# Kernel tuning notes

Hardware: AMD Instinct MI355X
Metric: run time of the kernel (lower is better)

The kernel has to match this reference:

```python
import jax, jax.numpy as jnp
import numpy as np

N_ATOM = 4_000_000
N_FRAG = 200_000
EIG_THRESHOLD = 0.01


def setup_inputs() -> dict:
    key = jax.random.key(0)
    k1, k2, k3, k4, k5 = jax.random.split(key, 5)
    f_atom = jax.random.normal(k1, (N_ATOM, 3), jnp.float32)
    atom_pos = jax.random.normal(k2, (N_ATOM, 3), jnp.float32) * 5.0
    T_frag = jax.random.normal(k3, (N_FRAG, 3), jnp.float32) * 5.0
    frag_id = jax.random.randint(k4, (N_ATOM,), 0, N_FRAG)
    frag_sizes = jax.random.randint(k5, (N_FRAG,), 1, 40)
    return {"f_atom": f_atom, "atom_pos": atom_pos, "T_frag": T_frag,
            "frag_id": frag_id, "frag_sizes": frag_sizes, "n_frag": N_FRAG}


def reference(f_atom, atom_pos, T_frag, frag_id, frag_sizes, n_frag):
    dtype = f_atom.dtype
    # scatter_mean(f_atom, frag_id): segment_sum / counts
    counts = jax.ops.segment_sum(jnp.ones((f_atom.shape[0],), dtype), frag_id,
                                 num_segments=n_frag)
    denom = jnp.maximum(counts, 1.0)[:, None]
    v_frag = jax.ops.segment_sum(f_atom, frag_id, num_segments=n_frag) / denom  # [F,3]

    r_arm = atom_pos - T_frag[frag_id]                                   # [N,3]
    torque = jax.ops.segment_sum(jnp.cross(r_arm, f_atom), frag_id,
                                 num_segments=n_frag)                    # [F,3]

    r2 = jnp.sum(r_arm * r_arm, axis=-1)                                 # [N]
    I_diag = jax.ops.segment_sum(r2, frag_id, num_segments=n_frag)       # [F]
    rr = r_arm[:, :, None] * r_arm[:, None, :]                           # [N,3,3]
    I_off = jax.ops.segment_sum(rr.reshape(-1, 9), frag_id,
                                num_segments=n_frag).reshape(-1, 3, 3)   # [F,3,3]
    I_tensor = I_diag[:, None, None] * jnp.eye(3, dtype=dtype) - I_off   # [F,3,3]

    eigenvalues, eigenvectors = jnp.linalg.eigh(I_tensor)                # [F,3], [F,3,3]
    max_eig = jnp.maximum(jnp.max(eigenvalues, axis=-1, keepdims=True), 1e-8)
    observable = (eigenvalues > EIG_THRESHOLD * max_eig).astype(dtype)   # [F,3]
    observable = jnp.where((frag_sizes <= 1)[:, None],
                           jnp.zeros((), dtype), observable)

    torque_eig = jnp.einsum('nji,nj->ni', eigenvectors, torque)          # V^T torque
    omega_eig = torque_eig / jnp.maximum(eigenvalues, 1e-6) * observable
    omega_frag = jnp.einsum('nij,nj->ni', eigenvectors, omega_eig)
    P_observable = jnp.einsum('nij,nj,nkj->nik', eigenvectors, observable, eigenvectors)
    return v_frag, omega_frag, P_observable
```

## Files before the change

kernel.cpp:

```cpp
#include <hip/hip_runtime.h>
#include <math.h>

__device__ __forceinline__ void frag_epilogue(
    const float* a, int f, int n_frag, const int* __restrict__ frag_sizes,
    float* __restrict__ out)
{
    float cntf  = a[12];
    float denom = fmaxf(cntf, 1.0f);
    float vfx = a[0] / denom, vfy = a[1] / denom, vfz = a[2] / denom;

    double tq0 = (double)a[3], tq1 = (double)a[4], tq2 = (double)a[5];
    double Mxx = (double)a[6], Myy = (double)a[7], Mzz = (double)a[8];
    double Mxy = (double)a[9], Mxz = (double)a[10], Myz = (double)a[11];
    double tr = Mxx + Myy + Mzz;

    double A[3][3] = {
        { tr - Mxx, -Mxy,     -Mxz     },
        { -Mxy,     tr - Myy, -Myz     },
        { -Mxz,     -Myz,     tr - Mzz }
    };
    double V[3][3] = {{1,0,0},{0,1,0},{0,0,1}};

    for (int sweep = 0; sweep < 6; ++sweep) {
        for (int pq = 0; pq < 3; ++pq) {
            int p = (pq == 2) ? 1 : 0;
            int q = (pq == 0) ? 1 : 2;
            double apq = A[p][q];
            if (fabs(apq) <= 1e-14 * (fabs(A[p][p]) + fabs(A[q][q])) ||
                fabs(apq) < 1e-300) continue;
            double theta = (A[q][q] - A[p][p]) / (2.0 * apq);
            double tt;
            if (fabs(theta) > 1e100) tt = 1.0 / (2.0 * theta);
            else tt = copysign(1.0, theta) / (fabs(theta) + sqrt(theta * theta + 1.0));
            double c = 1.0 / sqrt(tt * tt + 1.0);
            double s = tt * c;
            double app = A[p][p], aqq = A[q][q];
            A[p][p] = app - tt * apq;
            A[q][q] = aqq + tt * apq;
            A[p][q] = 0.0; A[q][p] = 0.0;
            int r = 3 - p - q;
            double arp = A[r][p], arq = A[r][q];
            A[r][p] = c * arp - s * arq; A[p][r] = A[r][p];
            A[r][q] = s * arp + c * arq; A[q][r] = A[r][q];
            for (int i2 = 0; i2 < 3; ++i2) {
                double vip = V[i2][p], viq = V[i2][q];
                V[i2][p] = c * vip - s * viq;
                V[i2][q] = s * vip + c * viq;
            }
        }
    }

    double lam0 = A[0][0], lam1 = A[1][1], lam2 = A[2][2];
    double maxeig = fmax(fmax(fmax(lam0, lam1), lam2), 1e-8);
    double thr = 0.01 * maxeig;
    bool small_frag = (frag_sizes[f] <= 1);
    double o0 = (!small_frag && lam0 > thr) ? 1.0 : 0.0;
    double o1 = (!small_frag && lam1 > thr) ? 1.0 : 0.0;
    double o2 = (!small_frag && lam2 > thr) ? 1.0 : 0.0;

    double te0 = V[0][0]*tq0 + V[1][0]*tq1 + V[2][0]*tq2;
    double te1 = V[0][1]*tq0 + V[1][1]*tq1 + V[2][1]*tq2;
    double te2 = V[0][2]*tq0 + V[1][2]*tq1 + V[2][2]*tq2;
    double we0 = te0 / fmax(lam0, 1e-6) * o0;
    double we1 = te1 / fmax(lam1, 1e-6) * o1;
    double we2 = te2 / fmax(lam2, 1e-6) * o2;
    double w0 = V[0][0]*we0 + V[0][1]*we1 + V[0][2]*we2;
    double w1 = V[1][0]*we0 + V[1][1]*we1 + V[1][2]*we2;
    double w2 = V[2][0]*we0 + V[2][1]*we1 + V[2][2]*we2;

    size_t F = (size_t)n_frag;
    out[(size_t)f*3 + 0] = vfx;
    out[(size_t)f*3 + 1] = vfy;
    out[(size_t)f*3 + 2] = vfz;
    out[F*3 + (size_t)f*3 + 0] = (float)w0;
    out[F*3 + (size_t)f*3 + 1] = (float)w1;
    out[F*3 + (size_t)f*3 + 2] = (float)w2;

    float* P = out + F*6 + (size_t)f*9;
    #pragma unroll
    for (int i2 = 0; i2 < 3; ++i2)
        #pragma unroll
        for (int k = 0; k < 3; ++k)
            P[i2*3 + k] = (float)(V[i2][0]*o0*V[k][0] + V[i2][1]*o1*V[k][1]
                                  + V[i2][2]*o2*V[k][2]);
}

#define NBK  512
#define FPB  400
#define CAP2 2048
#define TILE 16
#define APB  (256 * TILE)
#define MAXPT 8
#define NCHUNK 16
#define SCHUNK 2048
#define CPT    8

__global__ __launch_bounds__(256) void count_atoms(
    const int* __restrict__ frag_id,
    unsigned*  __restrict__ histrows,
    int n_atom)
{
    __shared__ unsigned hist[NBK];
    int t = threadIdx.x;
    for (int b = t; b < NBK; b += 256) hist[b] = 0;
    __syncthreads();
    const int4* fid4 = (const int4*)frag_id;
    int bs4 = blockIdx.x * (APB / 4);
    #pragma unroll
    for (int j = 0; j < TILE / 4; ++j) {
        int i4 = bs4 + j * 256 + t;
        if (4 * i4 < n_atom) {
            int4 v = fid4[i4];
            atomicAdd(&hist[v.x / FPB], 1u);
            atomicAdd(&hist[v.y / FPB], 1u);
            atomicAdd(&hist[v.z / FPB], 1u);
            atomicAdd(&hist[v.w / FPB], 1u);
        }
    }
    __syncthreads();
    unsigned* row = histrows + (size_t)blockIdx.x * NBK;
    for (int b = t; b < NBK; b += 256) row[b] = hist[b];
}

__global__ __launch_bounds__(256) void scan_pass1(
    const unsigned* __restrict__ histrows,
    unsigned* __restrict__ chunksums,
    int nblk, int ch)
{
    int col = blockIdx.x * 256 + threadIdx.x;
    int c   = blockIdx.y;
    int r0 = c * ch, r1 = r0 + ch;
    if (r1 > nblk) r1 = nblk;
    unsigned s = 0;
    for (int r = r0; r < r1; ++r) s += histrows[(size_t)r * NBK + col];
    chunksums[(size_t)c * NBK + col] = s;
}

__global__ __launch_bounds__(256) void scan_pass2(
    unsigned* __restrict__ chunksums,
    unsigned* __restrict__ totals)
{
    int col = blockIdx.x * 256 + threadIdx.x;
    unsigned cum = 0;
    #pragma unroll
    for (int c = 0; c < NCHUNK; ++c) {
        size_t idx = (size_t)c * NBK + col;
        unsigned v = chunksums[idx];
        chunksums[idx] = cum;
        cum += v;
    }
    totals[col] = cum;
}

__global__ __launch_bounds__(256) void scan_pass3(
    unsigned* __restrict__ histrows,
    const unsigned* __restrict__ chunksums,
    int nblk, int ch)
{
    int col = blockIdx.x * 256 + threadIdx.x;
    int c   = blockIdx.y;
    int r0 = c * ch, r1 = r0 + ch;
    if (r1 > nblk) r1 = nblk;
    unsigned cum = chunksums[(size_t)c * NBK + col];
    for (int r = r0; r < r1; ++r) {
        size_t idx = (size_t)r * NBK + col;
        unsigned v = histrows[idx];
        histrows[idx] = cum;
        cum += v;
    }
}

__global__ __launch_bounds__(256) void scan_base(
    const unsigned* __restrict__ totals,
    unsigned* __restrict__ bucket_base)
{
    __shared__ unsigned part[256];
    int t = threadIdx.x;
    unsigned v0 = totals[2*t], v1 = totals[2*t + 1];
    part[t] = v0 + v1;
    __syncthreads();
    for (int st = 1; st < 256; st <<= 1) {
        unsigned v = (t >= st) ? part[t - st] : 0u;
        __syncthreads();
        part[t] += v;
        __syncthreads();
    }
    unsigned base = (t == 0) ? 0u : part[t - 1];
    bucket_base[2*t]     = base;
    bucket_base[2*t + 1] = base + v0;
    if (t == 255) bucket_base[NBK] = part[255];
}

__global__ __launch_bounds__(256) void scatter_atoms(
    const float* __restrict__ f_atom,
    const float* __restrict__ atom_pos,
    const int*   __restrict__ frag_id,
    const unsigned* __restrict__ histrows,
    const unsigned* __restrict__ bucket_base,
    float4*      __restrict__ recs,
    int n_atom)
{
    __shared__ float    srt[SCHUNK * 7];
    __shared__ unsigned hist[NBK];
    __shared__ unsigned cbase[NBK];
    __shared__ unsigned obase[NBK];
    __shared__ unsigned sc[256];
    int t = threadIdx.x;

    const unsigned* row = histrows + (size_t)blockIdx.x * NBK;
    for (int b = t; b < NBK; b += 256) obase[b] = row[b] + bucket_base[b];

    const int4*   fid4 = (const int4*)frag_id;
    const float4* pos4 = (const float4*)atom_pos;
    const float4* ff4  = (const float4*)f_atom;
    int bs = blockIdx.x * APB;

    for (int c = 0; c < APB / SCHUNK; ++c) {
        int cs = bs + c * SCHUNK;
        int mchunk = n_atom - cs;
        if (mchunk > SCHUNK) mchunk = SCHUNK;
        if (mchunk < 0) mchunk = 0;

        for (int b = t; b < NBK; b += 256) hist[b] = 0;
        __syncthreads();

        int      bkv[CPT], lfv[CPT];
        unsigned rk[CPT];
        float ax[CPT], ay[CPT], az[CPT], gx[CPT], gy[CPT], gz[CPT];
        #pragma unroll
        for (int q = 0; q < CPT / 4; ++q) {
            int i4 = (cs >> 2) + q * 256 + t;
            if (4 * i4 < n_atom) {
                int4 v = fid4[i4];
                float4 p0 = pos4[3*(size_t)i4+0], p1 = pos4[3*(size_t)i4+1], p2 = pos4[3*(size_t)i4+2];
                float4 g0 = ff4[3*(size_t)i4+0],  g1 = ff4[3*(size_t)i4+1],  g2 = ff4[3*(size_t)i4+2];
                int   fid_[4] = {v.x, v.y, v.z, v.w};
                float px_[4] = {p0.x, p0.w, p1.z, p2.y};
                float py_[4] = {p0.y, p1.x, p1.w, p2.z};
                float pz_[4] = {p0.z, p1.y, p2.x, p2.w};
                float gx_[4] = {g0.x, g0.w, g1.z, g2.y};
                float gy_[4] = {g0.y, g1.x, g1.w, g2.z};
                float gz_[4] = {g0.z, g1.y, g2.x, g2.w};
                #pragma unroll
                for (int cc = 0; cc < 4; ++cc) {
                    int k = q * 4 + cc;
                    int fid = fid_[cc];
                    int bk = fid / FPB;
                    bkv[k] = bk;
                    lfv[k] = fid - bk * FPB;
                    rk[k]  = atomicAdd(&hist[bk], 1u);
                    ax[k] = px_[cc]; ay[k] = py_[cc]; az[k] = pz_[cc];
                    gx[k] = gx_[cc]; gy[k] = gy_[cc]; gz[k] = gz_[cc];
                }
            } else {
                #pragma unroll
                for (int cc = 0; cc < 4; ++cc) bkv[q * 4 + cc] = -1;
            }
        }
        __syncthreads();

        unsigned pv = hist[2*t] + hist[2*t + 1];
        sc[t] = pv;
        __syncthreads();
        #pragma unroll
        for (int st = 1; st < 256; st <<= 1) {
            unsigned v = (t >= st) ? sc[t - st] : 0u;
            __syncthreads();
            sc[t] += v;
            __syncthreads();
        }
        unsigned excl = sc[t] - pv;
        cbase[2*t]     = excl;
        cbase[2*t + 1] = excl + hist[2*t];
        __syncthreads();

        #pragma unroll
        for (int k = 0; k < CPT; ++k) {
            if (bkv[k] >= 0) {
                unsigned p = (cbase[bkv[k]] + rk[k]) * 7u;
                srt[p+0] = ax[k]; srt[p+1] = ay[k]; srt[p+2] = az[k];
                srt[p+3] = gx[k]; srt[p+4] = gy[k]; srt[p+5] = gz[k];
                srt[p+6] = __int_as_float(lfv[k] | (bkv[k] << 16));
            }
        }
        __syncthreads();

        #pragma unroll
        for (int k = 0; k < CPT; ++k) {
            int j = t + k * 256;
            if (j < mchunk) {
                const float* d = &srt[(unsigned)j * 7u];
                int pk = __float_as_int(d[6]);
                int lf = pk & 0xFFFF;
                int bk = pk >> 16;
                unsigned addr = obase[bk] + (unsigned)j - cbase[bk];
                recs[2*(size_t)addr + 0] = make_float4(d[0], d[1], d[2], __int_as_float(lf));
                recs[2*(size_t)addr + 1] = make_float4(d[3], d[4], d[5], 0.0f);
            }
        }
        __syncthreads();

        for (int b = t; b < NBK; b += 256) obase[b] += hist[b];
        __syncthreads();
    }
}

__global__ __launch_bounds__(256) void sort_reduce(
    const float4*   __restrict__ recs,
    const unsigned* __restrict__ bucket_base,
    const float*    __restrict__ T_frag,
    const int*      __restrict__ frag_sizes,
    float*          __restrict__ out,
    int n_frag)
{
    __shared__ float    srt[CAP2 * 7];
    __shared__ unsigned hist[FPB];
    __shared__ unsigned sc[256];
    __shared__ unsigned cbase[FPB];

    int b = blockIdx.x, t = threadIdx.x;
    int frag0 = b * FPB;
    int nf = n_frag - frag0;
    if (nf > FPB) nf = FPB;

    unsigned start = bucket_base[b];
    unsigned end   = bucket_base[b + 1];

    bool v0 = (t < nf);
    bool v1 = (256 + t < nf);
    float T0x=0,T0y=0,T0z=0, T1x=0,T1y=0,T1z=0;
    if (v0) { int f = frag0 + t;       T0x=T_frag[3*f]; T0y=T_frag[3*f+1]; T0z=T_frag[3*f+2]; }
    if (v1) { int f = frag0 + 256 + t; T1x=T_frag[3*f]; T1y=T_frag[3*f+1]; T1z=T_frag[3*f+2]; }

    float s0[12], s1[12];
    #pragma unroll
    for (int k = 0; k < 12; ++k) { s0[k] = 0.0f; s1[k] = 0.0f; }
    unsigned c0n = 0, c1n = 0;

    for (unsigned c0 = start; c0 < end; c0 += CAP2) {
        unsigned m = end - c0;
        if (m > CAP2) m = CAP2;

        for (int k = t; k < FPB; k += 256) hist[k] = 0;
        __syncthreads();

        float4 rv[MAXPT], fvv[MAXPT];
        int rlf[MAXPT];
        unsigned rrk[MAXPT];
        #pragma unroll
        for (int k = 0; k < MAXPT; ++k) {
            unsigned i = (unsigned)t + (unsigned)k * 256u;
            rlf[k] = -1;
            if (i < m) {
                rv[k]  = recs[2 * (size_t)(c0 + i) + 0];
                fvv[k] = recs[2 * (size_t)(c0 + i) + 1];
                int lf = __float_as_int(rv[k].w);
                rlf[k] = lf;
                rrk[k] = atomicAdd(&hist[lf], 1u);
            }
        }
        __syncthreads();

        unsigned p = 0;
        if (2 * t < FPB) p = hist[2*t] + hist[2*t + 1];
        sc[t] = p;
        __syncthreads();
        #pragma unroll
        for (int st = 1; st < 256; st <<= 1) {
            unsigned v = (t >= st) ? sc[t - st] : 0u;
            __syncthreads();
            sc[t] += v;
            __syncthreads();
        }
        if (2 * t < FPB) {
            unsigned excl = sc[t] - p;
            cbase[2*t]     = excl;
            cbase[2*t + 1] = excl + hist[2*t];
        }
        __syncthreads();

        #pragma unroll
        for (int k = 0; k < MAXPT; ++k) {
            if (rlf[k] >= 0) {
                unsigned q = (cbase[rlf[k]] + rrk[k]) * 7u;
                srt[q + 0] = rv[k].x;  srt[q + 1] = rv[k].y;  srt[q + 2] = rv[k].z;
                srt[q + 3] = fvv[k].x; srt[q + 4] = fvv[k].y; srt[q + 5] = fvv[k].z;
            }
        }
        __syncthreads();

        if (v0) {
            unsigned cb = cbase[t], cnt = hist[t];
            c0n += cnt;
            for (unsigned k = 0; k < cnt; ++k) {
                const float* d = &srt[(cb + k) * 7u];
                float rx = d[0] - T0x, ry = d[1] - T0y, rz = d[2] - T0z;
                float Fx = d[3], Fy = d[4], Fz = d[5];
                s0[0] += Fx; s0[1] += Fy; s0[2] += Fz;
                s0[3] += ry*Fz - rz*Fy;
                s0[4] += rz*Fx - rx*Fz;
                s0[5] += rx*Fy - ry*Fx;
                s0[6] += rx*rx; s0[7] += ry*ry; s0[8] += rz*rz;
                s0[9] += rx*ry; s0[10] += rx*rz; s0[11] += ry*rz;
            }
        }
        if (v1) {
            unsigned cb = cbase[256 + t], cnt = hist[256 + t];
            c1n += cnt;
            for (unsigned k = 0; k < cnt; ++k) {
                const float* d = &srt[(cb + k) * 7u];
                float rx = d[0] - T1x, ry = d[1] - T1y, rz = d[2] - T1z;
                float Fx = d[3], Fy = d[4], Fz = d[5];
                s1[0] += Fx; s1[1] += Fy; s1[2] += Fz;
                s1[3] += ry*Fz - rz*Fy;
                s1[4] += rz*Fx - rx*Fz;
                s1[5] += rx*Fy - ry*Fx;
                s1[6] += rx*rx; s1[7] += ry*ry; s1[8] += rz*rz;
                s1[9] += rx*ry; s1[10] += rx*rz; s1[11] += ry*rz;
            }
        }
        __syncthreads();
    }

    if (v0) {
        float a[13];
        #pragma unroll
        for (int k = 0; k < 12; ++k) a[k] = s0[k];
        a[12] = (float)c0n;
        frag_epilogue(a, frag0 + t, n_frag, frag_sizes, out);
    }
    if (v1) {
        float a[13];
        #pragma unroll
        for (int k = 0; k < 12; ++k) a[k] = s1[k];
        a[12] = (float)c1n;
        frag_epilogue(a, frag0 + 256 + t, n_frag, frag_sizes, out);
    }
}

#define NACC 16

__global__ __launch_bounds__(256) void atom_scatter_fb(
    const float* __restrict__ f_atom, const float* __restrict__ atom_pos,
    const float* __restrict__ T_frag, const int* __restrict__ frag_id,
    float* __restrict__ acc, int n_atom)
{
    int i = blockIdx.x * blockDim.x + threadIdx.x;
    if (i >= n_atom) return;
    int fid = frag_id[i];
    float fx = f_atom[3*i+0], fy = f_atom[3*i+1], fz = f_atom[3*i+2];
    float px = atom_pos[3*i+0], py = atom_pos[3*i+1], pz = atom_pos[3*i+2];
    float rx = px - T_frag[3*fid+0], ry = py - T_frag[3*fid+1], rz = pz - T_frag[3*fid+2];
    float cx = ry*fz - rz*fy, cy = rz*fx - rx*fz, cz = rx*fy - ry*fx;
    float* a = acc + (size_t)fid * NACC;
    atomicAdd(a+0, fx);    atomicAdd(a+1, fy);    atomicAdd(a+2, fz);
    atomicAdd(a+3, cx);    atomicAdd(a+4, cy);    atomicAdd(a+5, cz);
    atomicAdd(a+6, rx*rx); atomicAdd(a+7, ry*ry); atomicAdd(a+8, rz*rz);
    atomicAdd(a+9, rx*ry); atomicAdd(a+10, rx*rz); atomicAdd(a+11, ry*rz);
    atomicAdd(a+12, 1.0f);
}

__global__ __launch_bounds__(256) void frag_solve_fb(
    const float* __restrict__ acc, const int* __restrict__ frag_sizes,
    float* __restrict__ out, int n_frag)
{
    int f = blockIdx.x * blockDim.x + threadIdx.x;
    if (f >= n_frag) return;
    float a[13];
    #pragma unroll
    for (int k = 0; k < 13; ++k) a[k] = acc[(size_t)f * NACC + k];
    frag_epilogue(a, f, n_frag, frag_sizes, out);
}

extern "C" void kernel_launch(void* const* d_in, const int* in_sizes, int n_in,
                              void* d_out, int out_size, void* d_ws, size_t ws_size,
                              hipStream_t stream) {
    const float* f_atom     = (const float*)d_in[0];
    const float* atom_pos   = (const float*)d_in[1];
    const float* T_frag     = (const float*)d_in[2];
    const int*   frag_id    = (const int*)d_in[3];
    const int*   frag_sizes = (const int*)d_in[4];
    int n_atom = in_sizes[0] / 3;
    int n_frag = in_sizes[2] / 3;
    float* out = (float*)d_out;

    int nblk = (n_atom + APB - 1) / APB;
    int nbk  = (n_frag + FPB - 1) / FPB;
    int ch   = (nblk + NCHUNK - 1) / NCHUNK;

    size_t hist_bytes = (size_t)nblk * NBK * sizeof(unsigned);
    size_t cs_off     = hist_bytes;
    size_t tot_off    = cs_off + (size_t)NCHUNK * NBK * sizeof(unsigned);
    size_t base_off   = tot_off + NBK * sizeof(unsigned);
    size_t recs_off   = (base_off + (NBK + 1) * sizeof(unsigned) + 255) & ~(size_t)255;
    size_t need       = recs_off + (size_t)n_atom * 2 * sizeof(float4);

    if (ws_size >= need && nbk <= NBK && (n_atom % 4) == 0) {
        unsigned* histrows    = (unsigned*)d_ws;
        unsigned* chunksums   = (unsigned*)((char*)d_ws + cs_off);
        unsigned* totals      = (unsigned*)((char*)d_ws + tot_off);
        unsigned* bucket_base = (unsigned*)((char*)d_ws + base_off);
        float4*   recs        = (float4*)((char*)d_ws + recs_off);

        count_atoms<<<nblk, 256, 0, stream>>>(frag_id, histrows, n_atom);
        dim3 sgrid(NBK / 256, NCHUNK);
        scan_pass1<<<sgrid, 256, 0, stream>>>(histrows, chunksums, nblk, ch);
        scan_pass2<<<NBK / 256, 256, 0, stream>>>(chunksums, totals);
        scan_base<<<1, 256, 0, stream>>>(totals, bucket_base);
        scan_pass3<<<sgrid, 256, 0, stream>>>(histrows, chunksums, nblk, ch);
        scatter_atoms<<<nblk, 256, 0, stream>>>(
            f_atom, atom_pos, frag_id, histrows, bucket_base, recs, n_atom);
        sort_reduce<<<nbk, 256, 0, stream>>>(
            recs, bucket_base, T_frag, frag_sizes, out, n_frag);
    } else {
        float* acc = (float*)d_ws;
        hipMemsetAsync(acc, 0, (size_t)n_frag * NACC * sizeof(float), stream);
        atom_scatter_fb<<<(n_atom + 255) / 256, 256, 0, stream>>>(
            f_atom, atom_pos, T_frag, frag_id, acc, n_atom);
        frag_solve_fb<<<(n_frag + 255) / 256, 256, 0, stream>>>(acc, frag_sizes, out, n_frag);
    }
}
```

Baseline: 254.9 us.

## Replace per-chunk LDS counting sort with shared-memory float atomics in sort_reduce

The per-bucket kernel no longer sorts each chunk of records by local fragment through histogram, scan and LDS scatter, then reduces with one thread per fragment. Each of 512 threads now streams records and does 13 shared-memory float atomicAdds per atom into a per-fragment accumulator table, followed by the eigen epilogue. This drops several barriers and the scan, and fixes the load imbalance from uneven fragment sizes. In exchange it adds heavy LDS atomic traffic with contention on popular fragments, and the floating-point summation order becomes nondeterministic.

```diff
diff --git a/kernel.cpp b/kernel.cpp
--- a/kernel.cpp
+++ b/kernel.cpp
@@ -87,10 +87,8 @@
 
 #define NBK  512
 #define FPB  400
-#define CAP2 2048
 #define TILE 16
 #define APB  (256 * TILE)
-#define MAXPT 8
 #define NCHUNK 16
 #define SCHUNK 2048
 #define CPT    8
@@ -305,7 +303,7 @@
     }
 }
 
-__global__ __launch_bounds__(256) void sort_reduce(
+__global__ __launch_bounds__(512) void sort_reduce(
     const float4*   __restrict__ recs,
     const unsigned* __restrict__ bucket_base,
     const float*    __restrict__ T_frag,
@@ -313,128 +311,92 @@
     float*          __restrict__ out,
     int n_frag)
 {
-    __shared__ float    srt[CAP2 * 7];
-    __shared__ unsigned hist[FPB];
-    __shared__ unsigned sc[256];
-    __shared__ unsigned cbase[FPB];
+    __shared__ float  acc[13 * FPB];
+    __shared__ float4 Tl[FPB];
 
     int b = blockIdx.x, t = threadIdx.x;
     int frag0 = b * FPB;
     int nf = n_frag - frag0;
     if (nf > FPB) nf = FPB;
 
+    for (int k = t; k < 13 * FPB; k += 512) acc[k] = 0.0f;
+    for (int k = t; k < nf; k += 512) {
+        int f = frag0 + k;
+        Tl[k] = make_float4(T_frag[3*f+0], T_frag[3*f+1], T_frag[3*f+2], 0.0f);
+    }
+    __syncthreads();
+
     unsigned start = bucket_base[b];
     unsigned end   = bucket_base[b + 1];
 
-    bool v0 = (t < nf);
-    bool v1 = (256 + t < nf);
-    float T0x=0,T0y=0,T0z=0, T1x=0,T1y=0,T1z=0;
-    if (v0) { int f = frag0 + t;       T0x=T_frag[3*f]; T0y=T_frag[3*f+1]; T0z=T_frag[3*f+2]; }
-    if (v1) { int f = frag0 + 256 + t; T1x=T_frag[3*f]; T1y=T_frag[3*f+1]; T1z=T_frag[3*f+2]; }
-
-    float s0[12], s1[12];
-    #pragma unroll
-    for (int k = 0; k < 12; ++k) { s0[k] = 0.0f; s1[k] = 0.0f; }
-    unsigned c0n = 0, c1n = 0;
-
-    for (unsigned c0 = start; c0 < end; c0 += CAP2) {
-        unsigned m = end - c0;
-        if (m > CAP2) m = CAP2;
-
-        for (int k = t; k < FPB; k += 256) hist[k] = 0;
-        __syncthreads();
-
-        float4 rv[MAXPT], fvv[MAXPT];
-        int rlf[MAXPT];
-        unsigned rrk[MAXPT];
-        #pragma unroll
-        for (int k = 0; k < MAXPT; ++k) {
-            unsigned i = (unsigned)t + (unsigned)k * 256u;
-            rlf[k] = -1;
-            if (i < m) {
-                rv[k]  = recs[2 * (size_t)(c0 + i) + 0];
-                fvv[k] = recs[2 * (size_t)(c0 + i) + 1];
-                int lf = __float_as_int(rv[k].w);
-                rlf[k] = lf;
-                rrk[k] = atomicAdd(&hist[lf], 1u);
-            }
-        }
-        __syncthreads();
-
-        unsigned p = 0;
-        if (2 * t < FPB) p = hist[2*t] + hist[2*t + 1];
-        sc[t] = p;
-        __syncthreads();
-        #pragma unroll
-        for (int st = 1; st < 256; st <<= 1) {
-            unsigned v = (t >= st) ? sc[t - st] : 0u;
-            __syncthreads();
-            sc[t] += v;
-            __syncthreads();
-        }
-        if (2 * t < FPB) {
-            unsigned excl = sc[t] - p;
-            cbase[2*t]     = excl;
-            cbase[2*t + 1] = excl + hist[2*t];
-        }
-        __syncthreads();
-
-        #pragma unroll
-        for (int k = 0; k < MAXPT; ++k) {
-            if (rlf[k] >= 0) {
-                unsigned q = (cbase[rlf[k]] + rrk[k]) * 7u;
-                srt[q + 0] = rv[k].x;  srt[q + 1] = rv[k].y;  srt[q + 2] = rv[k].z;
-                srt[q + 3] = fvv[k].x; srt[q + 4] = fvv[k].y; srt[q + 5] = fvv[k].z;
-            }
-        }
-        __syncthreads();
-
-        if (v0) {
-            unsigned cb = cbase[t], cnt = hist[t];
-            c0n += cnt;
-            for (unsigned k = 0; k < cnt; ++k) {
-                const float* d = &srt[(cb + k) * 7u];
-                float rx = d[0] - T0x, ry = d[1] - T0y, rz = d[2] - T0z;
-                float Fx = d[3], Fy = d[4], Fz = d[5];
-                s0[0] += Fx; s0[1] += Fy; s0[2] += Fz;
-                s0[3] += ry*Fz - rz*Fy;
-                s0[4] += rz*Fx - rx*Fz;
-                s0[5] += rx*Fy - ry*Fx;
-                s0[6] += rx*rx; s0[7] += ry*ry; s0[8] += rz*rz;
-                s0[9] += rx*ry; s0[10] += rx*rz; s0[11] += ry*rz;
-            }
-        }
-        if (v1) {
-            unsigned cb = cbase[256 + t], cnt = hist[256 + t];
-            c1n += cnt;
-            for (unsigned k = 0; k < cnt; ++k) {
-                const float* d = &srt[(cb + k) * 7u];
-                float rx = d[0] - T1x, ry = d[1] - T1y, rz = d[2] - T1z;
-                float Fx = d[3], Fy = d[4], Fz = d[5];
-                s1[0] += Fx; s1[1] += Fy; s1[2] += Fz;
-                s1[3] += ry*Fz - rz*Fy;
-                s1[4] += rz*Fx - rx*Fz;
-                s1[5] += rx*Fy - ry*Fx;
-                s1[6] += rx*rx; s1[7] += ry*ry; s1[8] += rz*rz;
-                s1[9] += rx*ry; s1[10] += rx*rz; s1[11] += ry*rz;
-            }
-        }
-        __syncthreads();
-    }
-
-    if (v0) {
+    unsigned i = start + (unsigned)t;
+    for (; i + 512u < end; i += 1024u) {
+        float4 rv0 = recs[2*(size_t)i + 0];
+        float4 fv0 = recs[2*(size_t)i + 1];
+        float4 rv1 = recs[2*(size_t)(i + 512u) + 0];
+        float4 fv1 = recs[2*(size_t)(i + 512u) + 1];
+
+        int lf0 = __float_as_int(rv0.w);
+        float4 T0 = Tl[lf0];
+        float rx0 = rv0.x - T0.x, ry0 = rv0.y - T0.y, rz0 = rv0.z - T0.z;
+        atomicAdd(&acc[0*FPB+lf0], fv0.x);
+        atomicAdd(&acc[1*FPB+lf0], fv0.y);
+        atomicAdd(&acc[2*FPB+lf0], fv0.z);
+        atomicAdd(&acc[3*FPB+lf0], ry0*fv0.z - rz0*fv0.y);
+        atomicAdd(&acc[4*FPB+lf0], rz0*fv0.x - rx0*fv0.z);
+        atomicAdd(&acc[5*FPB+lf0], rx0*fv0.y - ry0*fv0.x);
+        atomicAdd(&acc[6*FPB+lf0], rx0*rx0);
+        atomicAdd(&acc[7*FPB+lf0], ry0*ry0);
+        atomicAdd(&acc[8*FPB+lf0], rz0*rz0);
+        atomicAdd(&acc[9*FPB+lf0], rx0*ry0);
+        atomicAdd(&acc[10*FPB+lf0], rx0*rz0);
+        atomicAdd(&acc[11*FPB+lf0], ry0*rz0);
+        atomicAdd(&acc[12*FPB+lf0], 1.0f);
+
+        int lf1 = __float_as_int(rv1.w);
+        float4 T1 = Tl[lf1];
+        float rx1 = rv1.x - T1.x, ry1 = rv1.y - T1.y, rz1 = rv1.z - T1.z;
+        atomicAdd(&acc[0*FPB+lf1], fv1.x);
+        atomicAdd(&acc[1*FPB+lf1], fv1.y);
+        atomicAdd(&acc[2*FPB+lf1], fv1.z);
+        atomicAdd(&acc[3*FPB+lf1], ry1*fv1.z - rz1*fv1.y);
+        atomicAdd(&acc[4*FPB+lf1], rz1*fv1.x - rx1*fv1.z);
+        atomicAdd(&acc[5*FPB+lf1], rx1*fv1.y - ry1*fv1.x);
+        atomicAdd(&acc[6*FPB+lf1], rx1*rx1);
+        atomicAdd(&acc[7*FPB+lf1], ry1*ry1);
+        atomicAdd(&acc[8*FPB+lf1], rz1*rz1);
+        atomicAdd(&acc[9*FPB+lf1], rx1*ry1);
+        atomicAdd(&acc[10*FPB+lf1], rx1*rz1);
+        atomicAdd(&acc[11*FPB+lf1], ry1*rz1);
+        atomicAdd(&acc[12*FPB+lf1], 1.0f);
+    }
+    for (; i < end; i += 512u) {
+        float4 rv = recs[2*(size_t)i + 0];
+        float4 fv = recs[2*(size_t)i + 1];
+        int lf = __float_as_int(rv.w);
+        float4 T0 = Tl[lf];
+        float rx = rv.x - T0.x, ry = rv.y - T0.y, rz = rv.z - T0.z;
+        atomicAdd(&acc[0*FPB+lf], fv.x);
+        atomicAdd(&acc[1*FPB+lf], fv.y);
+        atomicAdd(&acc[2*FPB+lf], fv.z);
+        atomicAdd(&acc[3*FPB+lf], ry*fv.z - rz*fv.y);
+        atomicAdd(&acc[4*FPB+lf], rz*fv.x - rx*fv.z);
+        atomicAdd(&acc[5*FPB+lf], rx*fv.y - ry*fv.x);
+        atomicAdd(&acc[6*FPB+lf], rx*rx);
+        atomicAdd(&acc[7*FPB+lf], ry*ry);
+        atomicAdd(&acc[8*FPB+lf], rz*rz);
+        atomicAdd(&acc[9*FPB+lf], rx*ry);
+        atomicAdd(&acc[10*FPB+lf], rx*rz);
+        atomicAdd(&acc[11*FPB+lf], ry*rz);
+        atomicAdd(&acc[12*FPB+lf], 1.0f);
+    }
+    __syncthreads();
+
+    for (int lf = t; lf < nf; lf += 512) {
         float a[13];
         #pragma unroll
-        for (int k = 0; k < 12; ++k) a[k] = s0[k];
-        a[12] = (float)c0n;
-        frag_epilogue(a, frag0 + t, n_frag, frag_sizes, out);
-    }
-    if (v1) {
-        float a[13];
-        #pragma unroll
-        for (int k = 0; k < 12; ++k) a[k] = s1[k];
-        a[12] = (float)c1n;
-        frag_epilogue(a, frag0 + 256 + t, n_frag, frag_sizes, out);
+        for (int c = 0; c < 13; ++c) a[c] = acc[c*FPB + lf];
+        frag_epilogue(a, frag0 + lf, n_frag, frag_sizes, out);
     }
 }
 
@@ -510,7 +472,7 @@
         scan_pass3<<<sgrid, 256, 0, stream>>>(histrows, chunksums, nblk, ch);
         scatter_atoms<<<nblk, 256, 0, stream>>>(
             f_atom, atom_pos, frag_id, histrows, bucket_base, recs, n_atom);
-        sort_reduce<<<nbk, 256, 0, stream>>>(
+        sort_reduce<<<nbk, 512, 0, stream>>>(
             recs, bucket_base, T_frag, frag_sizes, out, n_frag);
     } else {
         float* acc = (float*)d_ws;
```

New measurement: 479.5 us. 88.1% more time.

## Use 512-thread sort_reduce with one fragment per thread and wave-shuffle scan

Applied to the files above, without the earlier changes.

The sort_reduce kernel now launches 512 threads so each thread owns at most one fragment, instead of 256 threads each handling two fragments serially. The shared-memory chunk drops to 1024 records with 2 records per thread per pass. The 256-step barrier-heavy Hillis-Steele scan is replaced by a 64-lane shuffle scan plus a small cross-wave fixup. The aim is more parallelism in the reduction loop and far fewer barriers, at the cost of more chunk iterations per bucket and higher per-block thread and register pressure.

```diff
diff --git a/kernel.cpp b/kernel.cpp
--- a/kernel.cpp
+++ b/kernel.cpp
@@ -87,10 +87,10 @@
 
 #define NBK  512
 #define FPB  400
-#define CAP2 2048
+#define CAP2 1024
+#define MAXPT 2
 #define TILE 16
 #define APB  (256 * TILE)
-#define MAXPT 8
 #define NCHUNK 16
 #define SCHUNK 2048
 #define CPT    8
@@ -305,7 +305,7 @@
     }
 }
 
-__global__ __launch_bounds__(256) void sort_reduce(
+__global__ __launch_bounds__(512) void sort_reduce(
     const float4*   __restrict__ recs,
     const unsigned* __restrict__ bucket_base,
     const float*    __restrict__ T_frag,
@@ -315,10 +315,11 @@
 {
     __shared__ float    srt[CAP2 * 7];
     __shared__ unsigned hist[FPB];
-    __shared__ unsigned sc[256];
     __shared__ unsigned cbase[FPB];
+    __shared__ unsigned wsum[8];
 
     int b = blockIdx.x, t = threadIdx.x;
+    int lane = t & 63, w = t >> 6;
     int frag0 = b * FPB;
     int nf = n_frag - frag0;
     if (nf > FPB) nf = FPB;
@@ -326,22 +327,22 @@
     unsigned start = bucket_base[b];
     unsigned end   = bucket_base[b + 1];
 
-    bool v0 = (t < nf);
-    bool v1 = (256 + t < nf);
-    float T0x=0,T0y=0,T0z=0, T1x=0,T1y=0,T1z=0;
-    if (v0) { int f = frag0 + t;       T0x=T_frag[3*f]; T0y=T_frag[3*f+1]; T0z=T_frag[3*f+2]; }
-    if (v1) { int f = frag0 + 256 + t; T1x=T_frag[3*f]; T1y=T_frag[3*f+1]; T1z=T_frag[3*f+2]; }
-
-    float s0[12], s1[12];
+    bool own = (t < nf);
+    float Tx = 0, Ty = 0, Tz = 0;
+    if (own) {
+        int f = frag0 + t;
+        Tx = T_frag[3*f+0]; Ty = T_frag[3*f+1]; Tz = T_frag[3*f+2];
+    }
+    float s[12];
     #pragma unroll
-    for (int k = 0; k < 12; ++k) { s0[k] = 0.0f; s1[k] = 0.0f; }
-    unsigned c0n = 0, c1n = 0;
+    for (int k = 0; k < 12; ++k) s[k] = 0.0f;
+    unsigned fragcnt = 0;
 
     for (unsigned c0 = start; c0 < end; c0 += CAP2) {
         unsigned m = end - c0;
         if (m > CAP2) m = CAP2;
 
-        for (int k = t; k < FPB; k += 256) hist[k] = 0;
+        for (int k = t; k < FPB; k += 512) hist[k] = 0;
         __syncthreads();
 
         float4 rv[MAXPT], fvv[MAXPT];
@@ -349,7 +350,7 @@
         unsigned rrk[MAXPT];
         #pragma unroll
         for (int k = 0; k < MAXPT; ++k) {
-            unsigned i = (unsigned)t + (unsigned)k * 256u;
+            unsigned i = (unsigned)t + (unsigned)k * 512u;
             rlf[k] = -1;
             if (i < m) {
                 rv[k]  = recs[2 * (size_t)(c0 + i) + 0];
@@ -362,18 +363,25 @@
         __syncthreads();
 
         unsigned p = 0;
-        if (2 * t < FPB) p = hist[2*t] + hist[2*t + 1];
-        sc[t] = p;
-        __syncthreads();
-        #pragma unroll
-        for (int st = 1; st < 256; st <<= 1) {
-            unsigned v = (t >= st) ? sc[t - st] : 0u;
-            __syncthreads();
-            sc[t] += v;
-            __syncthreads();
-        }
-        if (2 * t < FPB) {
-            unsigned excl = sc[t] - p;
+        if (t < FPB / 2) p = hist[2*t] + hist[2*t + 1];
+        unsigned incl = p;
+        if (w < 4) {
+            #pragma unroll
+            for (int st = 1; st < 64; st <<= 1) {
+                unsigned v = __shfl_up(incl, (unsigned)st, 64);
+                if (lane >= st) incl += v;
+            }
+            if (lane == 63) wsum[w] = incl;
+        }
+        __syncthreads();
+        if (t == 0) {
+            unsigned c = 0;
+            #pragma unroll
+            for (int k = 0; k < 4; ++k) { unsigned v = wsum[k]; wsum[k] = c; c += v; }
+        }
+        __syncthreads();
+        if (t < FPB / 2) {
+            unsigned excl = incl - p + wsum[w];
             cbase[2*t]     = excl;
             cbase[2*t + 1] = excl + hist[2*t];
         }
@@ -389,52 +397,30 @@
         }
         __syncthreads();
 
-        if (v0) {
+        if (own) {
             unsigned cb = cbase[t], cnt = hist[t];
-            c0n += cnt;
+            fragcnt += cnt;
             for (unsigned k = 0; k < cnt; ++k) {
                 const float* d = &srt[(cb + k) * 7u];
-                float rx = d[0] - T0x, ry = d[1] - T0y, rz = d[2] - T0z;
+                float rx = d[0] - Tx, ry = d[1] - Ty, rz = d[2] - Tz;
                 float Fx = d[3], Fy = d[4], Fz = d[5];
-                s0[0] += Fx; s0[1] += Fy; s0[2] += Fz;
-                s0[3] += ry*Fz - rz*Fy;
-                s0[4] += rz*Fx - rx*Fz;
-                s0[5] += rx*Fy - ry*Fx;
-                s0[6] += rx*rx; s0[7] += ry*ry; s0[8] += rz*rz;
-                s0[9] += rx*ry; s0[10] += rx*rz; s0[11] += ry*rz;
-            }
-        }
-        if (v1) {
-            unsigned cb = cbase[256 + t], cnt = hist[256 + t];
-            c1n += cnt;
-            for (unsigned k = 0; k < cnt; ++k) {
-                const float* d = &srt[(cb + k) * 7u];
-                float rx = d[0] - T1x, ry = d[1] - T1y, rz = d[2] - T1z;
-                float Fx = d[3], Fy = d[4], Fz = d[5];
-                s1[0] += Fx; s1[1] += Fy; s1[2] += Fz;
-                s1[3] += ry*Fz - rz*Fy;
-                s1[4] += rz*Fx - rx*Fz;
-                s1[5] += rx*Fy - ry*Fx;
-                s1[6] += rx*rx; s1[7] += ry*ry; s1[8] += rz*rz;
-                s1[9] += rx*ry; s1[10] += rx*rz; s1[11] += ry*rz;
-            }
-        }
-        __syncthreads();
-    }
-
-    if (v0) {
+                s[0] += Fx; s[1] += Fy; s[2] += Fz;
+                s[3] += ry*Fz - rz*Fy;
+                s[4] += rz*Fx - rx*Fz;
+                s[5] += rx*Fy - ry*Fx;
+                s[6] += rx*rx; s[7] += ry*ry; s[8] += rz*rz;
+                s[9] += rx*ry; s[10] += rx*rz; s[11] += ry*rz;
+            }
+        }
+        __syncthreads();
+    }
+
+    if (own) {
         float a[13];
         #pragma unroll
-        for (int k = 0; k < 12; ++k) a[k] = s0[k];
-        a[12] = (float)c0n;
+        for (int k = 0; k < 12; ++k) a[k] = s[k];
+        a[12] = (float)fragcnt;
         frag_epilogue(a, frag0 + t, n_frag, frag_sizes, out);
-    }
-    if (v1) {
-        float a[13];
-        #pragma unroll
-        for (int k = 0; k < 12; ++k) a[k] = s1[k];
-        a[12] = (float)c1n;
-        frag_epilogue(a, frag0 + 256 + t, n_frag, frag_sizes, out);
     }
 }
 
@@ -510,7 +496,7 @@
         scan_pass3<<<sgrid, 256, 0, stream>>>(histrows, chunksums, nblk, ch);
         scatter_atoms<<<nblk, 256, 0, stream>>>(
             f_atom, atom_pos, frag_id, histrows, bucket_base, recs, n_atom);
-        sort_reduce<<<nbk, 256, 0, stream>>>(
+        sort_reduce<<<nbk, 512, 0, stream>>>(
             recs, bucket_base, T_frag, frag_sizes, out, n_frag);
     } else {
         float* acc = (float*)d_ws;
```

Measured after the change: 248.7 us. 1.02x faster.
